# Kernel tuning notes

Measured on AMD Instinct MI355X. Metric: run time of the kernel, lower is better.

The kernel has to match this reference:

```python
import jax, jax.numpy as jnp
import numpy as np

B, S, F, H, C = 64, 2048, 128, 256, 10


def setup_inputs() -> dict:
    key = jax.random.key(0)
    ks = jax.random.split(key, 11)
    s_in = 1.0 / np.sqrt(F)
    s_h = 1.0 / np.sqrt(H)
    return {
        "x": jax.random.normal(ks[0], (B, S, F), dtype=jnp.float32),
        "Wih0": jax.random.uniform(ks[1], (H, F), jnp.float32, -s_in, s_in),
        "Whh0": jax.random.uniform(ks[2], (H, H), jnp.float32, -s_h, s_h),
        "bih0": jax.random.uniform(ks[3], (H,), jnp.float32, -s_h, s_h),
        "bhh0": jax.random.uniform(ks[4], (H,), jnp.float32, -s_h, s_h),
        "Wih1": jax.random.uniform(ks[5], (H, H), jnp.float32, -s_h, s_h),
        "Whh1": jax.random.uniform(ks[6], (H, H), jnp.float32, -s_h, s_h),
        "bih1": jax.random.uniform(ks[7], (H,), jnp.float32, -s_h, s_h),
        "bhh1": jax.random.uniform(ks[8], (H,), jnp.float32, -s_h, s_h),
        "Wd": jax.random.uniform(ks[9], (C, H), jnp.float32, -s_h, s_h),
        "bd": jax.random.uniform(ks[10], (C,), jnp.float32, -s_h, s_h),
    }


def _rnn_layer(xs, Wih, Whh, bih, bhh):
    """Elman layer, batch_first xs: [B,S,Fin] -> [B,S,H].
    h_t = tanh(x_t @ Wih^T + bih + h_{t-1} @ Whh^T + bhh)
    """
    b, _, _ = xs.shape
    h = Whh.shape[0]
    # Precompute input projection for all timesteps in one big GEMM.
    xproj = jnp.einsum("bsf,hf->bsh", xs, Wih) + (bih + bhh)  # [B,S,H]

    def step(h_prev, xt):  # xt: [B,H]
        h_new = jnp.tanh(xt + h_prev @ Whh.T)
        return h_new, h_new

    h0 = jnp.zeros((b, h), xs.dtype)
    _, hs = jax.lax.scan(step, h0, jnp.swapaxes(xproj, 0, 1))  # [S,B,H]
    return jnp.swapaxes(hs, 0, 1)  # [B,S,H]


def reference(x, Wih0, Whh0, bih0, bhh0, Wih1, Whh1, bih1, bhh1, Wd, bd):
    h1 = _rnn_layer(x, Wih0, Whh0, bih0, bhh0)   # layer 0
    h2 = _rnn_layer(h1, Wih1, Whh1, bih1, bhh1)  # layer 1
    last = h2[:, -1, :]                          # many-to-one: last timestep
    return last @ Wd.T + bd                      # [B,C]
```

## Files before the change

### kernel.cpp

```cpp
#include <hip/hip_runtime.h>
#include <cstdint>
#include <cstddef>

#define BB 64
#define SS 2048
#define FF 128
#define HH 256
#define CC 10

typedef _Float16 f16;
typedef _Float16 f16x8 __attribute__((ext_vector_type(8)));
typedef _Float16 f16x4 __attribute__((ext_vector_type(4)));
typedef float f32x4 __attribute__((ext_vector_type(4)));

template<int K>
__global__ __launch_bounds__(256)
void xproj_gemm(const float* __restrict__ X, const float* __restrict__ W,
                const float* __restrict__ b1, const float* __restrict__ b2,
                f16* __restrict__ out)
{
    constexpr int BM = 64, BN = 64, BK = 32;
    __shared__ float As[BK][BM + 4];
    __shared__ float Ws[BK][BN + 4];

    const int m0 = blockIdx.x * BM;
    const int n0 = blockIdx.y * BN;
    const int tid = (int)threadIdx.x;
    const int tm = tid & 15;
    const int tn = tid >> 4;
    const int lr = tid >> 3;
    const int lc = tid & 7;

    float acc[4][4];
    #pragma unroll
    for (int i = 0; i < 4; ++i)
        #pragma unroll
        for (int jj = 0; jj < 4; ++jj) acc[i][jj] = 0.f;

    for (int k0 = 0; k0 < K; k0 += BK) {
        float4 a0 = *(const float4*)&X[(size_t)(m0 + lr) * K + k0 + lc * 4];
        float4 a1 = *(const float4*)&X[(size_t)(m0 + lr + 32) * K + k0 + lc * 4];
        float4 w0 = *(const float4*)&W[(size_t)(n0 + lr) * K + k0 + lc * 4];
        float4 w1 = *(const float4*)&W[(size_t)(n0 + lr + 32) * K + k0 + lc * 4];
        As[lc*4+0][lr]    = a0.x; As[lc*4+1][lr]    = a0.y; As[lc*4+2][lr]    = a0.z; As[lc*4+3][lr]    = a0.w;
        As[lc*4+0][lr+32] = a1.x; As[lc*4+1][lr+32] = a1.y; As[lc*4+2][lr+32] = a1.z; As[lc*4+3][lr+32] = a1.w;
        Ws[lc*4+0][lr]    = w0.x; Ws[lc*4+1][lr]    = w0.y; Ws[lc*4+2][lr]    = w0.z; Ws[lc*4+3][lr]    = w0.w;
        Ws[lc*4+0][lr+32] = w1.x; Ws[lc*4+1][lr+32] = w1.y; Ws[lc*4+2][lr+32] = w1.z; Ws[lc*4+3][lr+32] = w1.w;
        __syncthreads();
        #pragma unroll
        for (int k = 0; k < BK; ++k) {
            float4 av = *(const float4*)&As[k][tm * 4];
            float4 wv = *(const float4*)&Ws[k][tn * 4];
            acc[0][0] = fmaf(av.x, wv.x, acc[0][0]);
            acc[0][1] = fmaf(av.x, wv.y, acc[0][1]);
            acc[0][2] = fmaf(av.x, wv.z, acc[0][2]);
            acc[0][3] = fmaf(av.x, wv.w, acc[0][3]);
            acc[1][0] = fmaf(av.y, wv.x, acc[1][0]);
            acc[1][1] = fmaf(av.y, wv.y, acc[1][1]);
            acc[1][2] = fmaf(av.y, wv.z, acc[1][2]);
            acc[1][3] = fmaf(av.y, wv.w, acc[1][3]);
            acc[2][0] = fmaf(av.z, wv.x, acc[2][0]);
            acc[2][1] = fmaf(av.z, wv.y, acc[2][1]);
            acc[2][2] = fmaf(av.z, wv.z, acc[2][2]);
            acc[2][3] = fmaf(av.z, wv.w, acc[2][3]);
            acc[3][0] = fmaf(av.w, wv.x, acc[3][0]);
            acc[3][1] = fmaf(av.w, wv.y, acc[3][1]);
            acc[3][2] = fmaf(av.w, wv.z, acc[3][2]);
            acc[3][3] = fmaf(av.w, wv.w, acc[3][3]);
        }
        __syncthreads();
    }

    float4 bv1 = *(const float4*)&b1[n0 + tn * 4];
    float4 bv2 = *(const float4*)&b2[n0 + tn * 4];
    float bs0 = bv1.x + bv2.x, bs1 = bv1.y + bv2.y, bs2 = bv1.z + bv2.z, bs3 = bv1.w + bv2.w;
    #pragma unroll
    for (int i = 0; i < 4; ++i) {
        f16x4 o;
        o[0] = (f16)(acc[i][0] + bs0);
        o[1] = (f16)(acc[i][1] + bs1);
        o[2] = (f16)(acc[i][2] + bs2);
        o[3] = (f16)(acc[i][3] + bs3);
        *(f16x4*)&out[(size_t)(m0 + tm * 4 + i) * HH + n0 + tn * 4] = o;
    }
}

__global__ __launch_bounds__(256)
void xproj_gemm_f16(const f16* __restrict__ X, const float* __restrict__ W,
                    const float* __restrict__ b1, const float* __restrict__ b2,
                    f16* __restrict__ out)
{
    constexpr int K = HH, BM = 64, BN = 64, BK = 32;
    __shared__ float As[BK][BM + 4];
    __shared__ float Ws[BK][BN + 4];

    const int m0 = blockIdx.x * BM;
    const int n0 = blockIdx.y * BN;
    const int tid = (int)threadIdx.x;
    const int tm = tid & 15;
    const int tn = tid >> 4;
    const int ar = tid >> 2;
    const int ac = tid & 3;
    const int lr = tid >> 3;
    const int lc = tid & 7;

    float acc[4][4];
    #pragma unroll
    for (int i = 0; i < 4; ++i)
        #pragma unroll
        for (int jj = 0; jj < 4; ++jj) acc[i][jj] = 0.f;

    for (int k0 = 0; k0 < K; k0 += BK) {
        f16x8 a8 = *(const f16x8*)&X[(size_t)(m0 + ar) * K + k0 + ac * 8];
        float4 w0 = *(const float4*)&W[(size_t)(n0 + lr) * K + k0 + lc * 4];
        float4 w1 = *(const float4*)&W[(size_t)(n0 + lr + 32) * K + k0 + lc * 4];
        #pragma unroll
        for (int e = 0; e < 8; ++e) As[ac * 8 + e][ar] = (float)a8[e];
        Ws[lc*4+0][lr]    = w0.x; Ws[lc*4+1][lr]    = w0.y; Ws[lc*4+2][lr]    = w0.z; Ws[lc*4+3][lr]    = w0.w;
        Ws[lc*4+0][lr+32] = w1.x; Ws[lc*4+1][lr+32] = w1.y; Ws[lc*4+2][lr+32] = w1.z; Ws[lc*4+3][lr+32] = w1.w;
        __syncthreads();
        #pragma unroll
        for (int k = 0; k < BK; ++k) {
            float4 av = *(const float4*)&As[k][tm * 4];
            float4 wv = *(const float4*)&Ws[k][tn * 4];
            acc[0][0] = fmaf(av.x, wv.x, acc[0][0]);
            acc[0][1] = fmaf(av.x, wv.y, acc[0][1]);
            acc[0][2] = fmaf(av.x, wv.z, acc[0][2]);
            acc[0][3] = fmaf(av.x, wv.w, acc[0][3]);
            acc[1][0] = fmaf(av.y, wv.x, acc[1][0]);
            acc[1][1] = fmaf(av.y, wv.y, acc[1][1]);
            acc[1][2] = fmaf(av.y, wv.z, acc[1][2]);
            acc[1][3] = fmaf(av.y, wv.w, acc[1][3]);
            acc[2][0] = fmaf(av.z, wv.x, acc[2][0]);
            acc[2][1] = fmaf(av.z, wv.y, acc[2][1]);
            acc[2][2] = fmaf(av.z, wv.z, acc[2][2]);
            acc[2][3] = fmaf(av.z, wv.w, acc[2][3]);
            acc[3][0] = fmaf(av.w, wv.x, acc[3][0]);
            acc[3][1] = fmaf(av.w, wv.y, acc[3][1]);
            acc[3][2] = fmaf(av.w, wv.z, acc[3][2]);
            acc[3][3] = fmaf(av.w, wv.w, acc[3][3]);
        }
        __syncthreads();
    }

    float4 bv1 = *(const float4*)&b1[n0 + tn * 4];
    float4 bv2 = *(const float4*)&b2[n0 + tn * 4];
    float bs0 = bv1.x + bv2.x, bs1 = bv1.y + bv2.y, bs2 = bv1.z + bv2.z, bs3 = bv1.w + bv2.w;
    #pragma unroll
    for (int i = 0; i < 4; ++i) {
        f16x4 o;
        o[0] = (f16)(acc[i][0] + bs0);
        o[1] = (f16)(acc[i][1] + bs1);
        o[2] = (f16)(acc[i][2] + bs2);
        o[3] = (f16)(acc[i][3] + bs3);
        *(f16x4*)&out[(size_t)(m0 + tm * 4 + i) * HH + n0 + tn * 4] = o;
    }
}

__global__ __launch_bounds__(512, 2)
void rnn_scan_mfma(const f16* __restrict__ xproj,
                   const float* __restrict__ Whh,
                   f16* __restrict__ hout,
                   const float* __restrict__ Wd,
                   const float* __restrict__ bd,
                   float* __restrict__ outfinal,
                   int storeH)
{
    __shared__ __align__(16) f16 hbuf[2][16][HH];
    const int bg  = blockIdx.x;
    const int tid = (int)threadIdx.x;
    const int w   = tid >> 6;
    const int l   = tid & 63;
    const int l15 = l & 15;
    const int lq  = l >> 4;
    const int swz = (l15 & 7) << 4;

    f16x8 a[2][8];
    #pragma unroll
    for (int mt = 0; mt < 2; ++mt) {
        const int jrow = 32 * w + 16 * mt + l15;
        #pragma unroll
        for (int kt = 0; kt < 8; ++kt) {
            const float* src = Whh + (size_t)jrow * HH + 32 * kt + 8 * lq;
            float4 lo = *(const float4*)src;
            float4 hi = *(const float4*)(src + 4);
            f16x8 v;
            v[0] = (f16)lo.x; v[1] = (f16)lo.y; v[2] = (f16)lo.z; v[3] = (f16)lo.w;
            v[4] = (f16)hi.x; v[5] = (f16)hi.y; v[6] = (f16)hi.z; v[7] = (f16)hi.w;
            a[mt][kt] = v;
        }
    }

    for (int i = tid; i < 2048; i += 512) ((uint32_t*)hbuf)[i] = 0u;
    __syncthreads();

    const int j0base = 32 * w + 4 * lq;
    const f16* xpl = xproj + ((size_t)(bg * 16 + l15) * SS) * HH + j0base;
    f16* hol = storeH ? (hout + ((size_t)(bg * 16 + l15) * SS) * HH + j0base) : nullptr;

    f16x4 xq[4][2], xn[4][2];
    #pragma unroll
    for (int s = 0; s < 4; ++s)
        #pragma unroll
        for (int mt = 0; mt < 2; ++mt)
            xq[s][mt] = *(const f16x4*)(xpl + (size_t)s * HH + 16 * mt);

    int cur = 0;
    for (int t0 = 0; t0 < SS; t0 += 4) {
        const int tnb = (t0 + 4 < SS) ? (t0 + 4) : (SS - 4);
        #pragma unroll
        for (int s = 0; s < 4; ++s)
            #pragma unroll
            for (int mt = 0; mt < 2; ++mt)
                xn[s][mt] = *(const f16x4*)(xpl + (size_t)(tnb + s) * HH + 16 * mt);

        #pragma unroll
        for (int s = 0; s < 4; ++s) {
            const int t = t0 + s;
            f16x8 bfr[8];
            const char* hrow = (const char*)&hbuf[cur][l15][0];
            #pragma unroll
            for (int kt = 0; kt < 8; ++kt) {
                const int kb = (64 * kt + 16 * lq) ^ swz;
                bfr[kt] = *(const f16x8*)(hrow + kb);
            }

            f32x4 acc0[2], acc1[2];
            #pragma unroll
            for (int mt = 0; mt < 2; ++mt) {
                acc0[mt][0] = (float)xq[s][mt][0];
                acc0[mt][1] = (float)xq[s][mt][1];
                acc0[mt][2] = (float)xq[s][mt][2];
                acc0[mt][3] = (float)xq[s][mt][3];
                acc1[mt][0] = 0.f; acc1[mt][1] = 0.f;
                acc1[mt][2] = 0.f; acc1[mt][3] = 0.f;
            }
            #pragma unroll
            for (int kt = 0; kt < 4; ++kt)
                #pragma unroll
                for (int mt = 0; mt < 2; ++mt) {
                    acc0[mt] = __builtin_amdgcn_mfma_f32_16x16x32_f16(a[mt][kt],     bfr[kt],     acc0[mt], 0, 0, 0);
                    acc1[mt] = __builtin_amdgcn_mfma_f32_16x16x32_f16(a[mt][kt + 4], bfr[kt + 4], acc1[mt], 0, 0, 0);
                }

            #pragma unroll
            for (int mt = 0; mt < 2; ++mt) {
                f16x4 h4;
                #pragma unroll
                for (int r = 0; r < 4; ++r) {
                    float z = acc0[mt][r] + acc1[mt][r];
                    float e = __expf(2.0f * z);
                    float ht = 1.0f - 2.0f * __builtin_amdgcn_rcpf(e + 1.0f);
                    h4[r] = (f16)ht;
                }
                const int jb = (64 * w + 32 * mt + 8 * lq) ^ swz;
                *(f16x4*)((char*)&hbuf[cur ^ 1][l15][0] + jb) = h4;
                if (hol)
                    *(f16x4*)(hol + (size_t)t * HH + 16 * mt) = h4;
            }
            __syncthreads();
            cur ^= 1;
        }
        #pragma unroll
        for (int s = 0; s < 4; ++s)
            #pragma unroll
            for (int mt = 0; mt < 2; ++mt)
                xq[s][mt] = xn[s][mt];
    }

    if (outfinal != nullptr && tid < 16 * CC) {
        const int b = tid / CC, c = tid - CC * b;
        const int sw = (b & 7) << 4;
        const char* hrow = (const char*)&hbuf[cur][b][0];
        float accv = bd[c];
        for (int k = 0; k < HH; ++k) {
            f16 hv = *(const f16*)(hrow + ((2 * k) ^ sw));
            accv += (float)hv * Wd[(size_t)c * HH + k];
        }
        outfinal[(size_t)(bg * 16 + b) * CC + c] = accv;
    }
}

extern "C" void kernel_launch(void* const* d_in, const int* in_sizes, int n_in,
                              void* d_out, int out_size, void* d_ws, size_t ws_size,
                              hipStream_t stream)
{
    const float* x    = (const float*)d_in[0];
    const float* Wih0 = (const float*)d_in[1];
    const float* Whh0 = (const float*)d_in[2];
    const float* bih0 = (const float*)d_in[3];
    const float* bhh0 = (const float*)d_in[4];
    const float* Wih1 = (const float*)d_in[5];
    const float* Whh1 = (const float*)d_in[6];
    const float* bih1 = (const float*)d_in[7];
    const float* bhh1 = (const float*)d_in[8];
    const float* Wd   = (const float*)d_in[9];
    const float* bd   = (const float*)d_in[10];
    float* out = (float*)d_out;

    f16* xp = (f16*)d_ws;
    f16* h1 = xp + (size_t)BB * SS * HH;

    dim3 gemm_grid(BB * SS / 64, HH / 64);

    xproj_gemm<FF><<<gemm_grid, 256, 0, stream>>>(x, Wih0, bih0, bhh0, xp);
    rnn_scan_mfma<<<4, 512, 0, stream>>>(xp, Whh0, h1, nullptr, nullptr, nullptr, 1);

    xproj_gemm_f16<<<gemm_grid, 256, 0, stream>>>(h1, Wih1, bih1, bhh1, xp);
    rnn_scan_mfma<<<4, 512, 0, stream>>>(xp, Whh1, nullptr, Wd, bd, out, 0);
}
```

Measured before the change: 4.033 ms.

## Split RNN scan across twice as many blocks with eight batch rows each

Each scan block now handles 8 batch rows instead of 16, so the launch uses 8 blocks instead of 4. The 16 MFMA columns are filled with duplicated rows and only half the lanes write results. The XOR swizzle on the hidden-state buffer is replaced by padded rows (HH+8). The sequential scan is latency-bound, so spreading the batch over more CUs shortens each block's per-step work but wastes half of the MFMA throughput.

```diff
diff --git a/kernel.cpp b/kernel.cpp
--- a/kernel.cpp
+++ b/kernel.cpp
@@ -7,6 +7,7 @@
 #define FF 128
 #define HH 256
 #define CC 10
+#define HP (HH + 8)
 
 typedef _Float16 f16;
 typedef _Float16 f16x8 __attribute__((ext_vector_type(8)));
@@ -166,14 +167,14 @@
                    float* __restrict__ outfinal,
                    int storeH)
 {
-    __shared__ __align__(16) f16 hbuf[2][16][HH];
+    __shared__ __align__(16) f16 hbuf[2][8][HP];
     const int bg  = blockIdx.x;
     const int tid = (int)threadIdx.x;
     const int w   = tid >> 6;
     const int l   = tid & 63;
     const int l15 = l & 15;
+    const int b8  = l15 & 7;
     const int lq  = l >> 4;
-    const int swz = (l15 & 7) << 4;
 
     f16x8 a[2][8];
     #pragma unroll
@@ -191,12 +192,12 @@
         }
     }
 
-    for (int i = tid; i < 2048; i += 512) ((uint32_t*)hbuf)[i] = 0u;
+    for (int i = tid; i < 2 * 8 * HP / 2; i += 512) ((uint32_t*)hbuf)[i] = 0u;
     __syncthreads();
 
     const int j0base = 32 * w + 4 * lq;
-    const f16* xpl = xproj + ((size_t)(bg * 16 + l15) * SS) * HH + j0base;
-    f16* hol = storeH ? (hout + ((size_t)(bg * 16 + l15) * SS) * HH + j0base) : nullptr;
+    const f16* xpl = xproj + ((size_t)(bg * 8 + b8) * SS) * HH + j0base;
+    f16* hol = storeH ? (hout + ((size_t)(bg * 8 + b8) * SS) * HH + j0base) : nullptr;
 
     f16x4 xq[4][2], xn[4][2];
     #pragma unroll
@@ -218,12 +219,10 @@
         for (int s = 0; s < 4; ++s) {
             const int t = t0 + s;
             f16x8 bfr[8];
-            const char* hrow = (const char*)&hbuf[cur][l15][0];
-            #pragma unroll
-            for (int kt = 0; kt < 8; ++kt) {
-                const int kb = (64 * kt + 16 * lq) ^ swz;
-                bfr[kt] = *(const f16x8*)(hrow + kb);
-            }
+            const f16* hrow = &hbuf[cur][b8][0];
+            #pragma unroll
+            for (int kt = 0; kt < 8; ++kt)
+                bfr[kt] = *(const f16x8*)(hrow + 32 * kt + 8 * lq);
 
             f32x4 acc0[2], acc1[2];
             #pragma unroll
@@ -243,20 +242,21 @@
                     acc1[mt] = __builtin_amdgcn_mfma_f32_16x16x32_f16(a[mt][kt + 4], bfr[kt + 4], acc1[mt], 0, 0, 0);
                 }
 
-            #pragma unroll
-            for (int mt = 0; mt < 2; ++mt) {
-                f16x4 h4;
+            if (l15 < 8) {
                 #pragma unroll
-                for (int r = 0; r < 4; ++r) {
-                    float z = acc0[mt][r] + acc1[mt][r];
-                    float e = __expf(2.0f * z);
-                    float ht = 1.0f - 2.0f * __builtin_amdgcn_rcpf(e + 1.0f);
-                    h4[r] = (f16)ht;
+                for (int mt = 0; mt < 2; ++mt) {
+                    f16x4 h4;
+                    #pragma unroll
+                    for (int r = 0; r < 4; ++r) {
+                        float z = acc0[mt][r] + acc1[mt][r];
+                        float e = __expf(2.0f * z);
+                        float ht = 1.0f - 2.0f * __builtin_amdgcn_rcpf(e + 1.0f);
+                        h4[r] = (f16)ht;
+                    }
+                    *(f16x4*)(&hbuf[cur ^ 1][b8][0] + j0base + 16 * mt) = h4;
+                    if (hol)
+                        *(f16x4*)(hol + (size_t)t * HH + 16 * mt) = h4;
                 }
-                const int jb = (64 * w + 32 * mt + 8 * lq) ^ swz;
-                *(f16x4*)((char*)&hbuf[cur ^ 1][l15][0] + jb) = h4;
-                if (hol)
-                    *(f16x4*)(hol + (size_t)t * HH + 16 * mt) = h4;
             }
             __syncthreads();
             cur ^= 1;
@@ -268,16 +268,13 @@
                 xq[s][mt] = xn[s][mt];
     }
 
-    if (outfinal != nullptr && tid < 16 * CC) {
+    if (outfinal != nullptr && tid < 8 * CC) {
         const int b = tid / CC, c = tid - CC * b;
-        const int sw = (b & 7) << 4;
-        const char* hrow = (const char*)&hbuf[cur][b][0];
+        const f16* hrow = &hbuf[cur][b][0];
         float accv = bd[c];
-        for (int k = 0; k < HH; ++k) {
-            f16 hv = *(const f16*)(hrow + ((2 * k) ^ sw));
-            accv += (float)hv * Wd[(size_t)c * HH + k];
-        }
-        outfinal[(size_t)(bg * 16 + b) * CC + c] = accv;
+        for (int k = 0; k < HH; ++k)
+            accv += (float)hrow[k] * Wd[(size_t)c * HH + k];
+        outfinal[(size_t)(bg * 8 + b) * CC + c] = accv;
     }
 }
 
@@ -304,8 +301,8 @@
     dim3 gemm_grid(BB * SS / 64, HH / 64);
 
     xproj_gemm<FF><<<gemm_grid, 256, 0, stream>>>(x, Wih0, bih0, bhh0, xp);
-    rnn_scan_mfma<<<4, 512, 0, stream>>>(xp, Whh0, h1, nullptr, nullptr, nullptr, 1);
+    rnn_scan_mfma<<<8, 512, 0, stream>>>(xp, Whh0, h1, nullptr, nullptr, nullptr, 1);
 
     xproj_gemm_f16<<<gemm_grid, 256, 0, stream>>>(h1, Wih1, bih1, bhh1, xp);
-    rnn_scan_mfma<<<4, 512, 0, stream>>>(xp, Whh1, nullptr, Wd, bd, out, 0);
+    rnn_scan_mfma<<<8, 512, 0, stream>>>(xp, Whh1, nullptr, Wd, bd, out, 0);
 }
```

New measurement: 3.552 ms. 1.14x faster.
